# Optimization experiments

Hardware: AMD Instinct MI355X
Metric: run time of the kernel (lower is better)

The kernel has to match this reference:

```python
import jax, jax.numpy as jnp
import numpy as np

DIM = 1024
DEPTH = 3
BATCH = 8
SEQ = DIM  # module requires seq_len == dim for the residual add to broadcast


def setup_inputs() -> dict:
    key = jax.random.key(0)
    k1, k2, k3, k4 = jax.random.split(key, 4)
    x = jax.random.normal(k1, (BATCH, SEQ, DIM), dtype=jnp.float32)
    # torch.nn.Linear(dim, 3*dim): weight [3*dim, dim], bias [3*dim]
    Wqkv = jax.random.normal(k2, (3 * DIM, DIM), dtype=jnp.float32) * (1.0 / np.sqrt(DIM))
    bqkv = jax.random.normal(k3, (3 * DIM,), dtype=jnp.float32) * 0.01
    # self.w: Parameter of shape [depth, dim, dim], init randn
    w = jax.random.normal(k4, (DEPTH, DIM, DIM), dtype=jnp.float32)
    return {"x": x, "Wqkv": Wqkv, "bqkv": bqkv, "w": w}


def reference(x, Wqkv, bqkv, w):
    # qkv projection then chunk into q, k, v along last dim
    qkv = x @ Wqkv.T + bqkv                      # [B, S, 3*dim]
    q, k, v = jnp.split(qkv, 3, axis=-1)         # each [B, S, dim]
    scale = 1.0 / (q.shape[-1] ** 0.5)
    # sum over depth of (q @ w[i]) @ k^T, accumulated onto v
    # einsum contracts d (dim), e (dim), and sums over n (depth) in one pass
    scores = jnp.einsum('bsd,nde,bte->bst', q, w, k)  # [B, S, S]; requires S == dim
    return v + scores * scale
```

## Files before the change

kernel.cpp:

```cpp
#include <hip/hip_runtime.h>
#include <hip/hip_bf16.h>
#include <stdint.h>

typedef __bf16 bf16_t;
typedef __bf16 bf16x8 __attribute__((ext_vector_type(8)));
typedef __bf16 bf16x4 __attribute__((ext_vector_type(4)));
typedef float  f32x4  __attribute__((ext_vector_type(4)));

#define DIM   1024
#define BATCH 8
#define NTOK  (BATCH * DIM)
#define SCALE 0.03125f

__global__ __launch_bounds__(256)
void k_prep(const float* __restrict__ x, const float* __restrict__ Wqkv,
            const float* __restrict__ w,
            bf16_t* __restrict__ xb, bf16_t* __restrict__ wbig,
            bf16_t* __restrict__ wtb, bf16_t* __restrict__ wqt)
{
    __shared__ float tile[32][33];
    const int b = blockIdx.x;
    if (b < 8192) {
        const int i = b * 256 + threadIdx.x;
        const float4 v = reinterpret_cast<const float4*>(x)[i];
        bf16x4 o;
        o.x = (bf16_t)v.x; o.y = (bf16_t)v.y; o.z = (bf16_t)v.z; o.w = (bf16_t)v.w;
        reinterpret_cast<bf16x4*>(xb)[i] = o;
    } else if (b < 10240) {
        const int i = (b - 8192) * 256 + threadIdx.x;
        const float4 v = reinterpret_cast<const float4*>(Wqkv + 1048576)[i];
        bf16x4 o;
        o.x = (bf16_t)v.x; o.y = (bf16_t)v.y; o.z = (bf16_t)v.z; o.w = (bf16_t)v.w;
        reinterpret_cast<bf16x4*>(wbig + 1048576)[i] = o;
    } else if (b < 11264) {
        const int t  = b - 10240;
        const int tx = threadIdx.x & 31, ty = threadIdx.x >> 5;
        const int d0 = (t & 31) * 32, e0 = (t >> 5) * 32;
#pragma unroll
        for (int r = 0; r < 4; ++r) {
            const int d = d0 + r * 8 + ty;
            const int e = e0 + tx;
            tile[r * 8 + ty][tx] =
                w[d * 1024 + e] + w[1048576 + d * 1024 + e] + w[2097152 + d * 1024 + e];
        }
        __syncthreads();
#pragma unroll
        for (int r = 0; r < 4; ++r) {
            const int e = e0 + r * 8 + ty;
            const int d = d0 + tx;
            wtb[e * 1024 + d] = (bf16_t)tile[tx][r * 8 + ty];
        }
    } else {
        const int t  = b - 11264;
        const int tx = threadIdx.x & 31, ty = threadIdx.x >> 5;
        const int e0 = (t & 31) * 32, d0 = (t >> 5) * 32;
#pragma unroll
        for (int r = 0; r < 4; ++r)
            tile[r * 8 + ty][tx] = Wqkv[(long)(e0 + r * 8 + ty) * 1024 + d0 + tx];
        __syncthreads();
#pragma unroll
        for (int r = 0; r < 4; ++r)
            wqt[(long)(d0 + r * 8 + ty) * 1024 + e0 + tx] = (bf16_t)tile[tx][r * 8 + ty];
    }
}

__global__ __launch_bounds__(256)
void k_mid(const float* __restrict__ bq, const bf16_t* __restrict__ wtb,
           const bf16_t* __restrict__ wqt, float* __restrict__ bqwO,
           float* __restrict__ oP)
{
    __shared__ __align__(16) bf16_t As[128 * 32];
    __shared__ __align__(16) bf16_t Bs[128 * 32];

    const int tid  = threadIdx.x;
    const int wave = tid >> 6;
    const int lane = tid & 63;

    if (blockIdx.x < 256) {
        const int n = blockIdx.x * 4 + wave;
        const bf16_t* row = wtb + (long)n * 1024;
        float s = 0.f;
#pragma unroll
        for (int c = 0; c < 2; ++c) {
            const int d0 = (lane + c * 64) * 8;
            const bf16x8 v = *reinterpret_cast<const bf16x8*>(row + d0);
#pragma unroll
            for (int e = 0; e < 8; ++e) s += bq[d0 + e] * (float)v[e];
        }
#pragma unroll
        for (int off = 32; off; off >>= 1) s += __shfl_down(s, off);
        if (lane == 0) bqwO[n] = s;
        return;
    }

    const int s  = blockIdx.x - 256;
    const int bm = (s >> 5) * 128;
    const int bn = ((s >> 2) & 7) * 128;
    const int kb = (s & 3) * 256;
    float* outP  = oP + (long)(s & 3) * 1048576;
    const int wr = wave >> 1, wc = wave & 1;
    const int lhi = lane >> 4, llo = lane & 15;

    f32x4 acc[4][4];
    const f32x4 fz = {0.f, 0.f, 0.f, 0.f};
#pragma unroll
    for (int i = 0; i < 4; ++i)
#pragma unroll
        for (int j = 0; j < 4; ++j) acc[i][j] = fz;

    for (int k0 = 0; k0 < 256; k0 += 32) {
#pragma unroll
        for (int i = 0; i < 2; ++i) {
            const int c  = wave * 128 + i * 64 + lane;
            const int r  = c >> 2;
            const int cc = (c & 3) << 3;
            const long ga = (long)(bm + r) * 1024 + kb + k0 + cc;
            const long gb = (long)(bn + r) * 1024 + kb + k0 + cc;
            const int lbase = (wave * 128 + i * 64) << 3;
            __builtin_amdgcn_global_load_lds(
                (const __attribute__((address_space(1))) uint32_t*)(wtb + ga),
                (__attribute__((address_space(3))) uint32_t*)(&As[lbase]), 16, 0, 0);
            __builtin_amdgcn_global_load_lds(
                (const __attribute__((address_space(1))) uint32_t*)(wqt + gb),
                (__attribute__((address_space(3))) uint32_t*)(&Bs[lbase]), 16, 0, 0);
        }
        __syncthreads();

        bf16x8 af[4], bfr[4];
#pragma unroll
        for (int mi = 0; mi < 4; ++mi)
            af[mi] = *reinterpret_cast<const bf16x8*>(&As[(wr * 64 + mi * 16 + llo) * 32 + lhi * 8]);
#pragma unroll
        for (int ni = 0; ni < 4; ++ni)
            bfr[ni] = *reinterpret_cast<const bf16x8*>(&Bs[(wc * 64 + ni * 16 + llo) * 32 + lhi * 8]);
#pragma unroll
        for (int mi = 0; mi < 4; ++mi)
#pragma unroll
            for (int ni = 0; ni < 4; ++ni)
                acc[mi][ni] = __builtin_amdgcn_mfma_f32_16x16x32_bf16(af[mi], bfr[ni], acc[mi][ni], 0, 0, 0);
        __syncthreads();
    }

#pragma unroll
    for (int mi = 0; mi < 4; ++mi) {
        const int r0 = bm + wr * 64 + mi * 16 + lhi * 4;
#pragma unroll
        for (int ni = 0; ni < 4; ++ni) {
            const int cg = bn + wc * 64 + ni * 16 + llo;
            const f32x4 v = acc[mi][ni];
#pragma unroll
            for (int j = 0; j < 4; ++j)
                outP[(long)(r0 + j) * 1024 + cg] = v[j];
        }
    }
}

__global__ __launch_bounds__(256)
void k_cvt4(const float* __restrict__ p, bf16_t* __restrict__ out) {
    const int i = blockIdx.x * 256 + threadIdx.x;
    const f32x4* rp = reinterpret_cast<const f32x4*>(p);
    const f32x4 a = rp[i];
    const f32x4 b = rp[i + 262144];
    const f32x4 c = rp[i + 524288];
    const f32x4 d = rp[i + 786432];
    bf16x4 o;
    o.x = (bf16_t)(a.x + b.x + c.x + d.x);
    o.y = (bf16_t)(a.y + b.y + c.y + d.y);
    o.z = (bf16_t)(a.z + b.z + c.z + d.z);
    o.w = (bf16_t)(a.w + b.w + c.w + d.w);
    reinterpret_cast<bf16x4*>(out)[i] = o;
}

template<int BN_, int MODE>
__global__ __launch_bounds__(512, 2)
void k_db(const bf16_t* __restrict__ A, const bf16_t* __restrict__ Bp,
          const float* __restrict__ bqw, const float* __restrict__ bqkv,
          bf16_t* __restrict__ oQW, bf16_t* __restrict__ oK, float* __restrict__ oF)
{
    constexpr int NF   = BN_ / 64;
    constexpr int LB   = BN_ / 64;
    constexpr int LPT  = 2 + LB;
    constexpr int SLOT = (128 + BN_) * 128;
    constexpr int NTT  = 16;
    __shared__ __align__(16) unsigned char slds[2 * SLOT];

    const int tid  = threadIdx.x;
    const int wave = tid >> 6, lane = tid & 63;
    const int wm = wave >> 2, wn = wave & 3;
    const int llo = lane & 15, lhi = lane >> 4;

    int bm, bn; long zz = 0;
    if (MODE == 1) {
        bm = blockIdx.x * 128; bn = blockIdx.y * BN_;
    } else {
        const int nw = ((int)blockIdx.x & 7) * 64 + ((int)blockIdx.x >> 3);
        zz = (long)(nw >> 6) << 20;
        const int r = nw & 63;
        bm = (r >> 3) * 128; bn = (r & 7) * 128;
    }

    const bf16_t* sp[LPT]; int dst[LPT];
#pragma unroll
    for (int j = 0; j < 2; ++j) {
        const int C = j * 512 + tid;
        const int r = C >> 3, u = (C & 7) ^ (r & 7);
        sp[j] = A + zz + (long)(bm + r) * 1024 + (u << 3);
        dst[j] = C << 4;
    }
#pragma unroll
    for (int j = 0; j < LB; ++j) {
        const int C = j * 512 + tid;
        const int r = C >> 3, u = (C & 7) ^ (r & 7);
        sp[2 + j] = Bp + zz + (long)(bn + r) * 1024 + (u << 3);
        dst[2 + j] = 16384 + (C << 4);
    }

    auto stage = [&](int tt) {
        unsigned char* s = &slds[(tt & 1) * SLOT];
        const long ko = (long)tt << 6;
#pragma unroll
        for (int j = 0; j < LPT; ++j)
            __builtin_amdgcn_global_load_lds(
                (const __attribute__((address_space(1))) uint32_t*)(sp[j] + ko),
                (__attribute__((address_space(3))) uint32_t*)(s + dst[j]), 16, 0, 0);
    };

    f32x4 acc[4][NF];
    const f32x4 fz = {0.f, 0.f, 0.f, 0.f};
#pragma unroll
    for (int i = 0; i < 4; ++i)
#pragma unroll
        for (int j = 0; j < NF; ++j) acc[i][j] = fz;

    stage(0);

    for (int t = 0; t < NTT; ++t) {
        if (t + 1 < NTT) {
            stage(t + 1);
            asm volatile("s_waitcnt vmcnt(%0)" :: "i"(LPT) : "memory");
        } else {
            asm volatile("s_waitcnt vmcnt(0)" ::: "memory");
        }
        __builtin_amdgcn_s_barrier();

        const unsigned char* sb = &slds[(t & 1) * SLOT];
#pragma unroll
        for (int ks = 0; ks < 2; ++ks) {
            bf16x8 af[4], bfv[NF];
#pragma unroll
            for (int mi = 0; mi < 4; ++mi) {
                const int r = wm * 64 + mi * 16 + llo;
                af[mi] = *reinterpret_cast<const bf16x8*>(
                    sb + r * 128 + ((((ks << 2) | lhi) ^ (r & 7)) << 4));
            }
#pragma unroll
            for (int ni = 0; ni < NF; ++ni) {
                const int r = wn * (NF * 16) + ni * 16 + llo;
                bfv[ni] = *reinterpret_cast<const bf16x8*>(
                    sb + 16384 + r * 128 + ((((ks << 2) | lhi) ^ (r & 7)) << 4));
            }
            __builtin_amdgcn_s_setprio(1);
#pragma unroll
            for (int mi = 0; mi < 4; ++mi)
#pragma unroll
                for (int ni = 0; ni < NF; ++ni)
                    acc[mi][ni] = __builtin_amdgcn_mfma_f32_16x16x32_bf16(
                        af[mi], bfv[ni], acc[mi][ni], 0, 0, 0);
            __builtin_amdgcn_s_setprio(0);
        }
        asm volatile("s_waitcnt lgkmcnt(0)" ::: "memory");
        __builtin_amdgcn_s_barrier();
    }

#pragma unroll
    for (int mi = 0; mi < 4; ++mi) {
        const long r0 = bm + wm * 64 + mi * 16 + lhi * 4;
#pragma unroll
        for (int ni = 0; ni < NF; ++ni) {
            const int cg = bn + wn * (NF * 16) + ni * 16 + llo;
            const f32x4 v = acc[mi][ni];
            if (MODE == 1) {
                const int sec = cg >> 10;
                const int c1  = cg & 1023;
                const float bb = (sec == 0) ? bqw[cg] : bqkv[cg];
#pragma unroll
                for (int j = 0; j < 4; ++j) {
                    const long idx = (r0 + j) * 1024 + c1;
                    const float val = v[j] + bb;
                    if (sec == 0)      oQW[idx] = (bf16_t)val;
                    else if (sec == 1) oK[idx] = (bf16_t)val;
                    else               oF[idx] = val;
                }
            } else {
#pragma unroll
                for (int j = 0; j < 4; ++j) {
                    const long idx = zz + (r0 + j) * 1024 + cg;
                    oF[idx] = oF[idx] + SCALE * v[j];
                }
            }
        }
    }
}

extern "C" void kernel_launch(void* const* d_in, const int* in_sizes, int n_in,
                              void* d_out, int out_size, void* d_ws, size_t ws_size,
                              hipStream_t stream) {
    const float* x    = (const float*)d_in[0];
    const float* Wqkv = (const float*)d_in[1];
    const float* bqkv = (const float*)d_in[2];
    const float* w    = (const float*)d_in[3];
    float* out = (float*)d_out;

    char* ws = (char*)d_ws;
    bf16_t* xb   = (bf16_t*)(ws);
    bf16_t* wbig = (bf16_t*)(ws + (16l << 20));
    float*  bqw  = (float*) (ws + (22l << 20));
    bf16_t* kb   = (bf16_t*)(ws + (22l << 20) + 65536);
    float*  part = (float*) kb;
    bf16_t* qwb  = (bf16_t*)(ws + (38l << 20) + 65536);
    bf16_t* wtb  = qwb;
    bf16_t* wqt  = qwb + 1048576;
    if (ws_size < (size_t)(54l << 20) + 65536) return;

    k_prep<<<12288, 256, 0, stream>>>(x, Wqkv, w, xb, wbig, wtb, wqt);

    k_mid<<<512, 256, 0, stream>>>(bqkv, wtb, wqt, bqw, part);

    k_cvt4<<<1024, 256, 0, stream>>>(part, wbig);

    k_db<192, 1><<<dim3(64, 16), 512, 0, stream>>>(xb, wbig, bqw, bqkv, qwb, kb, out);

    k_db<128, 2><<<dim3(512), 512, 0, stream>>>(qwb, kb, nullptr, nullptr,
                                                nullptr, nullptr, out);
}
```

Measured before the change: 109.1 us.

## Reassociate score chain into a fused Wq^T·Weff·Wk matrix with rank-1 bias terms

Instead of projecting Q (folded with the summed depth weight), K and V and then multiplying QW by K^T, the code precomputes M = Wq^T·Weff·Wk with two small split-K GEMMs. It then computes T = x·M and forms scores plus V in one concatenated-K GEMM ([T | x] × [x | Wv]^T). Bias interactions are folded into per-row and per-column vectors (RU, RW, cO) and added in the epilogue. The goal is to cut total GEMM FLOPs and drop the separate K and QW intermediates, at the cost of more launches, extra rounding through a bf16 M, and altered numerics.

Result: slower. 112.2 us (+2.8%).

```diff
diff --git a/kernel.cpp b/kernel.cpp
--- a/kernel.cpp
+++ b/kernel.cpp
@@ -9,14 +9,96 @@
 
 #define DIM   1024
 #define BATCH 8
-#define NTOK  (BATCH * DIM)
 #define SCALE 0.03125f
+
+
+__device__ __forceinline__ float rowdot_bf16(const bf16_t* __restrict__ row,
+                                             const float* __restrict__ vec, int lane) {
+    float s = 0.f;
+#pragma unroll
+    for (int c = 0; c < 2; ++c) {
+        const int d0 = (lane + c * 64) * 8;
+        const bf16x8 v = *reinterpret_cast<const bf16x8*>(row + d0);
+#pragma unroll
+        for (int e = 0; e < 8; ++e) s += vec[d0 + e] * (float)v[e];
+    }
+#pragma unroll
+    for (int off = 32; off; off >>= 1) s += __shfl_down(s, off);
+    return s;
+}
+
+__device__ __forceinline__ void gemm_sk(const bf16_t* __restrict__ A, const bf16_t* __restrict__ B,
+                                        float* __restrict__ oP, int s, int tid,
+                                        bf16_t* As, bf16_t* Bs)
+{
+    const int wave = tid >> 6, lane = tid & 63;
+    const int bm = (s >> 5) * 128;
+    const int bn = ((s >> 2) & 7) * 128;
+    const int kb = (s & 3) * 256;
+    float* outP  = oP + (long)(s & 3) * 1048576;
+    const int wr = wave >> 1, wc = wave & 1;
+    const int lhi = lane >> 4, llo = lane & 15;
+
+    f32x4 acc[4][4];
+    const f32x4 fz = {0.f, 0.f, 0.f, 0.f};
+#pragma unroll
+    for (int i = 0; i < 4; ++i)
+#pragma unroll
+        for (int j = 0; j < 4; ++j) acc[i][j] = fz;
+
+    for (int k0 = 0; k0 < 256; k0 += 32) {
+#pragma unroll
+        for (int i = 0; i < 2; ++i) {
+            const int c  = wave * 128 + i * 64 + lane;
+            const int r  = c >> 2;
+            const int cc = (c & 3) << 3;
+            const long ga = (long)(bm + r) * 1024 + kb + k0 + cc;
+            const long gb = (long)(bn + r) * 1024 + kb + k0 + cc;
+            const int lbase = (wave * 128 + i * 64) << 3;
+            __builtin_amdgcn_global_load_lds(
+                (const __attribute__((address_space(1))) uint32_t*)(A + ga),
+                (__attribute__((address_space(3))) uint32_t*)(&As[lbase]), 16, 0, 0);
+            __builtin_amdgcn_global_load_lds(
+                (const __attribute__((address_space(1))) uint32_t*)(B + gb),
+                (__attribute__((address_space(3))) uint32_t*)(&Bs[lbase]), 16, 0, 0);
+        }
+        __syncthreads();
+
+        bf16x8 af[4], bfr[4];
+#pragma unroll
+        for (int mi = 0; mi < 4; ++mi)
+            af[mi] = *reinterpret_cast<const bf16x8*>(&As[(wr * 64 + mi * 16 + llo) * 32 + lhi * 8]);
+#pragma unroll
+        for (int ni = 0; ni < 4; ++ni)
+            bfr[ni] = *reinterpret_cast<const bf16x8*>(&Bs[(wc * 64 + ni * 16 + llo) * 32 + lhi * 8]);
+#pragma unroll
+        for (int mi = 0; mi < 4; ++mi)
+#pragma unroll
+            for (int ni = 0; ni < 4; ++ni)
+                acc[mi][ni] = __builtin_amdgcn_mfma_f32_16x16x32_bf16(af[mi], bfr[ni], acc[mi][ni], 0, 0, 0);
+        __syncthreads();
+    }
+
+#pragma unroll
+    for (int mi = 0; mi < 4; ++mi) {
+        const int r0 = bm + wr * 64 + mi * 16 + lhi * 4;
+#pragma unroll
+        for (int ni = 0; ni < 4; ++ni) {
+            const int cg = bn + wc * 64 + ni * 16 + llo;
+            const f32x4 v = acc[mi][ni];
+#pragma unroll
+            for (int j = 0; j < 4; ++j)
+                outP[(long)(r0 + j) * 1024 + cg] = v[j];
+        }
+    }
+}
 
 __global__ __launch_bounds__(256)
 void k_prep(const float* __restrict__ x, const float* __restrict__ Wqkv,
             const float* __restrict__ w,
-            bf16_t* __restrict__ xb, bf16_t* __restrict__ wbig,
-            bf16_t* __restrict__ wtb, bf16_t* __restrict__ wqt)
+            bf16_t* __restrict__ xb, bf16_t* __restrict__ wvb,
+            bf16_t* __restrict__ weff, bf16_t* __restrict__ wtb,
+            bf16_t* __restrict__ wqt, bf16_t* __restrict__ wkt)
 {
     __shared__ float tile[32][33];
     const int b = blockIdx.x;
@@ -26,162 +108,173 @@
         bf16x4 o;
         o.x = (bf16_t)v.x; o.y = (bf16_t)v.y; o.z = (bf16_t)v.z; o.w = (bf16_t)v.w;
         reinterpret_cast<bf16x4*>(xb)[i] = o;
-    } else if (b < 10240) {
+    } else if (b < 9216) {
         const int i = (b - 8192) * 256 + threadIdx.x;
-        const float4 v = reinterpret_cast<const float4*>(Wqkv + 1048576)[i];
+        const float4 v = reinterpret_cast<const float4*>(Wqkv + 2097152)[i];
         bf16x4 o;
         o.x = (bf16_t)v.x; o.y = (bf16_t)v.y; o.z = (bf16_t)v.z; o.w = (bf16_t)v.w;
-        reinterpret_cast<bf16x4*>(wbig + 1048576)[i] = o;
-    } else if (b < 11264) {
-        const int t  = b - 10240;
+        reinterpret_cast<bf16x4*>(wvb)[i] = o;
+    } else if (b < 10240) {
+        const int t  = b - 9216;
         const int tx = threadIdx.x & 31, ty = threadIdx.x >> 5;
         const int d0 = (t & 31) * 32, e0 = (t >> 5) * 32;
 #pragma unroll
         for (int r = 0; r < 4; ++r) {
             const int d = d0 + r * 8 + ty;
             const int e = e0 + tx;
-            tile[r * 8 + ty][tx] =
+            const float sum =
                 w[d * 1024 + e] + w[1048576 + d * 1024 + e] + w[2097152 + d * 1024 + e];
+            tile[r * 8 + ty][tx] = sum;
+            weff[(long)d * 1024 + e] = (bf16_t)sum;
         }
         __syncthreads();
 #pragma unroll
         for (int r = 0; r < 4; ++r) {
             const int e = e0 + r * 8 + ty;
             const int d = d0 + tx;
-            wtb[e * 1024 + d] = (bf16_t)tile[tx][r * 8 + ty];
+            wtb[(long)e * 1024 + d] = (bf16_t)tile[tx][r * 8 + ty];
         }
     } else {
-        const int t  = b - 11264;
+        const bool isQ = (b < 11264);
+        const int t  = b - (isQ ? 10240 : 11264);
+        const float* src = isQ ? Wqkv : (Wqkv + 1048576);
+        bf16_t* dst = isQ ? wqt : wkt;
         const int tx = threadIdx.x & 31, ty = threadIdx.x >> 5;
         const int e0 = (t & 31) * 32, d0 = (t >> 5) * 32;
 #pragma unroll
         for (int r = 0; r < 4; ++r)
-            tile[r * 8 + ty][tx] = Wqkv[(long)(e0 + r * 8 + ty) * 1024 + d0 + tx];
+            tile[r * 8 + ty][tx] = src[(long)(e0 + r * 8 + ty) * 1024 + d0 + tx];
         __syncthreads();
 #pragma unroll
         for (int r = 0; r < 4; ++r)
-            wqt[(long)(d0 + r * 8 + ty) * 1024 + e0 + tx] = (bf16_t)tile[tx][r * 8 + ty];
+            dst[(long)(d0 + r * 8 + ty) * 1024 + e0 + tx] = (bf16_t)tile[tx][r * 8 + ty];
     }
 }
 
 __global__ __launch_bounds__(256)
-void k_mid(const float* __restrict__ bq, const bf16_t* __restrict__ wtb,
-           const bf16_t* __restrict__ wqt, float* __restrict__ bqwO,
-           float* __restrict__ oP)
+void k_midA(const bf16_t* __restrict__ wkt, const bf16_t* __restrict__ weff,
+            const bf16_t* __restrict__ wtb, const float* __restrict__ bqkv,
+            float* __restrict__ pX1, float* __restrict__ h1, float* __restrict__ h2)
 {
     __shared__ __align__(16) bf16_t As[128 * 32];
     __shared__ __align__(16) bf16_t Bs[128 * 32];
-
-    const int tid  = threadIdx.x;
-    const int wave = tid >> 6;
-    const int lane = tid & 63;
-
     if (blockIdx.x < 256) {
-        const int n = blockIdx.x * 4 + wave;
-        const bf16_t* row = wtb + (long)n * 1024;
-        float s = 0.f;
-#pragma unroll
-        for (int c = 0; c < 2; ++c) {
-            const int d0 = (lane + c * 64) * 8;
-            const bf16x8 v = *reinterpret_cast<const bf16x8*>(row + d0);
-#pragma unroll
-            for (int e = 0; e < 8; ++e) s += bq[d0 + e] * (float)v[e];
-        }
-#pragma unroll
-        for (int off = 32; off; off >>= 1) s += __shfl_down(s, off);
-        if (lane == 0) bqwO[n] = s;
+        gemm_sk(wkt, weff, pX1, blockIdx.x, threadIdx.x, As, Bs);
         return;
     }
-
-    const int s  = blockIdx.x - 256;
-    const int bm = (s >> 5) * 128;
-    const int bn = ((s >> 2) & 7) * 128;
-    const int kb = (s & 3) * 256;
-    float* outP  = oP + (long)(s & 3) * 1048576;
-    const int wr = wave >> 1, wc = wave & 1;
-    const int lhi = lane >> 4, llo = lane & 15;
-
-    f32x4 acc[4][4];
-    const f32x4 fz = {0.f, 0.f, 0.f, 0.f};
-#pragma unroll
-    for (int i = 0; i < 4; ++i)
-#pragma unroll
-        for (int j = 0; j < 4; ++j) acc[i][j] = fz;
-
-    for (int k0 = 0; k0 < 256; k0 += 32) {
-#pragma unroll
-        for (int i = 0; i < 2; ++i) {
-            const int c  = wave * 128 + i * 64 + lane;
-            const int r  = c >> 2;
-            const int cc = (c & 3) << 3;
-            const long ga = (long)(bm + r) * 1024 + kb + k0 + cc;
-            const long gb = (long)(bn + r) * 1024 + kb + k0 + cc;
-            const int lbase = (wave * 128 + i * 64) << 3;
-            __builtin_amdgcn_global_load_lds(
-                (const __attribute__((address_space(1))) uint32_t*)(wtb + ga),
-                (__attribute__((address_space(3))) uint32_t*)(&As[lbase]), 16, 0, 0);
-            __builtin_amdgcn_global_load_lds(
-                (const __attribute__((address_space(1))) uint32_t*)(wqt + gb),
-                (__attribute__((address_space(3))) uint32_t*)(&Bs[lbase]), 16, 0, 0);
-        }
-        __syncthreads();
-
-        bf16x8 af[4], bfr[4];
-#pragma unroll
-        for (int mi = 0; mi < 4; ++mi)
-            af[mi] = *reinterpret_cast<const bf16x8*>(&As[(wr * 64 + mi * 16 + llo) * 32 + lhi * 8]);
-#pragma unroll
-        for (int ni = 0; ni < 4; ++ni)
-            bfr[ni] = *reinterpret_cast<const bf16x8*>(&Bs[(wc * 64 + ni * 16 + llo) * 32 + lhi * 8]);
-#pragma unroll
-        for (int mi = 0; mi < 4; ++mi)
-#pragma unroll
-            for (int ni = 0; ni < 4; ++ni)
-                acc[mi][ni] = __builtin_amdgcn_mfma_f32_16x16x32_bf16(af[mi], bfr[ni], acc[mi][ni], 0, 0, 0);
-        __syncthreads();
-    }
-
-#pragma unroll
-    for (int mi = 0; mi < 4; ++mi) {
-        const int r0 = bm + wr * 64 + mi * 16 + lhi * 4;
-#pragma unroll
-        for (int ni = 0; ni < 4; ++ni) {
-            const int cg = bn + wc * 64 + ni * 16 + llo;
-            const f32x4 v = acc[mi][ni];
-#pragma unroll
-            for (int j = 0; j < 4; ++j)
-                outP[(long)(r0 + j) * 1024 + cg] = v[j];
-        }
+    const int wave = threadIdx.x >> 6, lane = threadIdx.x & 63;
+    const int r = ((int)blockIdx.x - 256) * 4 + wave;
+    if (r < 1024) {
+        const float s = rowdot_bf16(weff + (long)r * 1024, bqkv + 1024, lane);
+        if (lane == 0) h1[r] = s;
+    } else {
+        const float s = rowdot_bf16(wtb + (long)(r - 1024) * 1024, bqkv, lane);
+        if (lane == 0) h2[r - 1024] = s;
     }
 }
 
 __global__ __launch_bounds__(256)
-void k_cvt4(const float* __restrict__ p, bf16_t* __restrict__ out) {
+void k_cvtA(const float* __restrict__ p, bf16_t* __restrict__ X1b,
+            const bf16_t* __restrict__ wqt, const bf16_t* __restrict__ wkt,
+            const float* __restrict__ h1, const float* __restrict__ h2,
+            const float* __restrict__ bqkv,
+            float* __restrict__ u, float* __restrict__ w2, float* __restrict__ cO)
+{
+    const int b = blockIdx.x;
+    if (b < 1024) {
+        const int i = b * 256 + threadIdx.x;
+        const f32x4* rp = reinterpret_cast<const f32x4*>(p);
+        const f32x4 a0 = rp[i], a1 = rp[i + 262144], a2 = rp[i + 524288], a3 = rp[i + 786432];
+        bf16x4 o;
+        o.x = (bf16_t)(a0.x + a1.x + a2.x + a3.x);
+        o.y = (bf16_t)(a0.y + a1.y + a2.y + a3.y);
+        o.z = (bf16_t)(a0.z + a1.z + a2.z + a3.z);
+        o.w = (bf16_t)(a0.w + a1.w + a2.w + a3.w);
+        reinterpret_cast<bf16x4*>(X1b)[i] = o;
+    } else if (b < 1536) {
+        const int wave = threadIdx.x >> 6, lane = threadIdx.x & 63;
+        const int rr = (b - 1024) * 4 + wave;
+        if (rr < 1024) {
+            const float s = rowdot_bf16(wqt + (long)rr * 1024, h1, lane);
+            if (lane == 0) u[rr] = s;
+        } else {
+            const float s = rowdot_bf16(wkt + (long)(rr - 1024) * 1024, h2, lane);
+            if (lane == 0) w2[rr - 1024] = s;
+        }
+    } else {
+        if (threadIdx.x < 64) {
+            float s = 0.f;
+            for (int i = threadIdx.x; i < 1024; i += 64) s += bqkv[i] * h1[i];
+#pragma unroll
+            for (int off = 32; off; off >>= 1) s += __shfl_down(s, off);
+            if (threadIdx.x == 0) cO[0] = s;
+        }
+    }
+}
+
+__global__ __launch_bounds__(256)
+void k_midB(const bf16_t* __restrict__ X1b, const bf16_t* __restrict__ wqt,
+            float* __restrict__ pMT, const bf16_t* __restrict__ xb,
+            const float* __restrict__ u, const float* __restrict__ w2,
+            const float* __restrict__ cO,
+            float* __restrict__ RU, float* __restrict__ RW)
+{
+    __shared__ __align__(16) bf16_t As[128 * 32];
+    __shared__ __align__(16) bf16_t Bs[128 * 32];
+    if (blockIdx.x < 256) {
+        gemm_sk(X1b, wqt, pMT, blockIdx.x, threadIdx.x, As, Bs);
+        return;
+    }
+    const int wave = threadIdx.x >> 6, lane = threadIdx.x & 63;
+    const int s = ((int)blockIdx.x - 256) * 4 + wave;
+    const bf16_t* row = xb + (long)s * 1024;
+    float s1 = 0.f, s2 = 0.f;
+#pragma unroll
+    for (int c = 0; c < 2; ++c) {
+        const int d0 = (lane + c * 64) * 8;
+        const bf16x8 v = *reinterpret_cast<const bf16x8*>(row + d0);
+#pragma unroll
+        for (int e = 0; e < 8; ++e) {
+            const float f = (float)v[e];
+            s1 += u[d0 + e] * f;
+            s2 += w2[d0 + e] * f;
+        }
+    }
+#pragma unroll
+    for (int off = 32; off; off >>= 1) { s1 += __shfl_down(s1, off); s2 += __shfl_down(s2, off); }
+    if (lane == 0) {
+        RU[s] = SCALE * (s1 + cO[0]);
+        RW[s] = SCALE * s2;
+    }
+}
+
+__global__ __launch_bounds__(256)
+void k_cvtS(const float* __restrict__ p, bf16_t* __restrict__ out) {
     const int i = blockIdx.x * 256 + threadIdx.x;
     const f32x4* rp = reinterpret_cast<const f32x4*>(p);
-    const f32x4 a = rp[i];
-    const f32x4 b = rp[i + 262144];
-    const f32x4 c = rp[i + 524288];
-    const f32x4 d = rp[i + 786432];
+    const f32x4 a0 = rp[i], a1 = rp[i + 262144], a2 = rp[i + 524288], a3 = rp[i + 786432];
     bf16x4 o;
-    o.x = (bf16_t)(a.x + b.x + c.x + d.x);
-    o.y = (bf16_t)(a.y + b.y + c.y + d.y);
-    o.z = (bf16_t)(a.z + b.z + c.z + d.z);
-    o.w = (bf16_t)(a.w + b.w + c.w + d.w);
+    o.x = (bf16_t)(SCALE * (a0.x + a1.x + a2.x + a3.x));
+    o.y = (bf16_t)(SCALE * (a0.y + a1.y + a2.y + a3.y));
+    o.z = (bf16_t)(SCALE * (a0.z + a1.z + a2.z + a3.z));
+    o.w = (bf16_t)(SCALE * (a0.w + a1.w + a2.w + a3.w));
     reinterpret_cast<bf16x4*>(out)[i] = o;
 }
 
-template<int BN_, int MODE>
+#define GLOAD(SRC, DST) __builtin_amdgcn_global_load_lds( \
+    (const __attribute__((address_space(1))) uint32_t*)(SRC), \
+    (__attribute__((address_space(3))) uint32_t*)(DST), 16, 0, 0)
+
+template<int MODE>
 __global__ __launch_bounds__(512, 2)
-void k_db(const bf16_t* __restrict__ A, const bf16_t* __restrict__ Bp,
-          const float* __restrict__ bqw, const float* __restrict__ bqkv,
-          bf16_t* __restrict__ oQW, bf16_t* __restrict__ oK, float* __restrict__ oF)
-{
-    constexpr int NF   = BN_ / 64;
-    constexpr int LB   = BN_ / 64;
-    constexpr int LPT  = 2 + LB;
-    constexpr int SLOT = (128 + BN_) * 128;
-    constexpr int NTT  = 16;
+void k_db2(const bf16_t* __restrict__ A1, const bf16_t* __restrict__ A2,
+           const bf16_t* __restrict__ B1, const bf16_t* __restrict__ B2,
+           const float* __restrict__ RUv, const float* __restrict__ RWv,
+           const float* __restrict__ bv,
+           bf16_t* __restrict__ oT, float* __restrict__ oF)
+{
+    constexpr int SLOT = 32768;
+    constexpr int NTT  = (MODE == 0) ? 16 : 32;
     __shared__ __align__(16) unsigned char slds[2 * SLOT];
 
     const int tid  = threadIdx.x;
@@ -189,55 +282,55 @@
     const int wm = wave >> 2, wn = wave & 3;
     const int llo = lane & 15, lhi = lane >> 4;
 
-    int bm, bn; long zz = 0;
-    if (MODE == 1) {
-        bm = blockIdx.x * 128; bn = blockIdx.y * BN_;
+    int bm, bn, z = 0;
+    if (MODE == 0) {
+        bm = ((int)blockIdx.x >> 3) * 128;
+        bn = ((int)blockIdx.x & 7) * 128;
     } else {
         const int nw = ((int)blockIdx.x & 7) * 64 + ((int)blockIdx.x >> 3);
-        zz = (long)(nw >> 6) << 20;
+        z = nw >> 6;
         const int r = nw & 63;
         bm = (r >> 3) * 128; bn = (r & 7) * 128;
     }
-
-    const bf16_t* sp[LPT]; int dst[LPT];
+    const long zo = (long)z << 20;
+
+    const bf16_t *sA1[2], *sB1[2], *sA2[2], *sB2[2];
+    int dA[2], dB[2];
 #pragma unroll
     for (int j = 0; j < 2; ++j) {
         const int C = j * 512 + tid;
         const int r = C >> 3, u = (C & 7) ^ (r & 7);
-        sp[j] = A + zz + (long)(bm + r) * 1024 + (u << 3);
-        dst[j] = C << 4;
-    }
-#pragma unroll
-    for (int j = 0; j < LB; ++j) {
-        const int C = j * 512 + tid;
-        const int r = C >> 3, u = (C & 7) ^ (r & 7);
-        sp[2 + j] = Bp + zz + (long)(bn + r) * 1024 + (u << 3);
-        dst[2 + j] = 16384 + (C << 4);
+        const long aoff = (long)(bm + r) * 1024 + (u << 3);
+        const long boff = (long)(bn + r) * 1024 + (u << 3);
+        sA1[j] = A1 + zo + aoff;  dA[j] = C << 4;
+        sB1[j] = B1 + zo + boff;  dB[j] = 16384 + (C << 4);
+        if (MODE == 1) { sA2[j] = A2 + zo + aoff; sB2[j] = B2 + boff; }
     }
 
     auto stage = [&](int tt) {
         unsigned char* s = &slds[(tt & 1) * SLOT];
-        const long ko = (long)tt << 6;
-#pragma unroll
-        for (int j = 0; j < LPT; ++j)
-            __builtin_amdgcn_global_load_lds(
-                (const __attribute__((address_space(1))) uint32_t*)(sp[j] + ko),
-                (__attribute__((address_space(3))) uint32_t*)(s + dst[j]), 16, 0, 0);
+        const long ko = (long)(tt & 15) << 6;
+        const bool hB = (MODE == 1) && (tt >= 16);
+#pragma unroll
+        for (int j = 0; j < 2; ++j) {
+            GLOAD((hB ? sA2[j] : sA1[j]) + ko, s + dA[j]);
+            GLOAD((hB ? sB2[j] : sB1[j]) + ko, s + dB[j]);
+        }
     };
 
-    f32x4 acc[4][NF];
+    f32x4 acc[4][2];
     const f32x4 fz = {0.f, 0.f, 0.f, 0.f};
 #pragma unroll
     for (int i = 0; i < 4; ++i)
 #pragma unroll
-        for (int j = 0; j < NF; ++j) acc[i][j] = fz;
+        for (int j = 0; j < 2; ++j) acc[i][j] = fz;
 
     stage(0);
 
     for (int t = 0; t < NTT; ++t) {
         if (t + 1 < NTT) {
             stage(t + 1);
-            asm volatile("s_waitcnt vmcnt(%0)" :: "i"(LPT) : "memory");
+            asm volatile("s_waitcnt vmcnt(4)" ::: "memory");
         } else {
             asm volatile("s_waitcnt vmcnt(0)" ::: "memory");
         }
@@ -246,7 +339,7 @@
         const unsigned char* sb = &slds[(t & 1) * SLOT];
 #pragma unroll
         for (int ks = 0; ks < 2; ++ks) {
-            bf16x8 af[4], bfv[NF];
+            bf16x8 af[4], bfv[2];
 #pragma unroll
             for (int mi = 0; mi < 4; ++mi) {
                 const int r = wm * 64 + mi * 16 + llo;
@@ -254,8 +347,8 @@
                     sb + r * 128 + ((((ks << 2) | lhi) ^ (r & 7)) << 4));
             }
 #pragma unroll
-            for (int ni = 0; ni < NF; ++ni) {
-                const int r = wn * (NF * 16) + ni * 16 + llo;
+            for (int ni = 0; ni < 2; ++ni) {
+                const int r = wn * 32 + ni * 16 + llo;
                 bfv[ni] = *reinterpret_cast<const bf16x8*>(
                     sb + 16384 + r * 128 + ((((ks << 2) | lhi) ^ (r & 7)) << 4));
             }
@@ -263,7 +356,7 @@
 #pragma unroll
             for (int mi = 0; mi < 4; ++mi)
 #pragma unroll
-                for (int ni = 0; ni < NF; ++ni)
+                for (int ni = 0; ni < 2; ++ni)
                     acc[mi][ni] = __builtin_amdgcn_mfma_f32_16x16x32_bf16(
                         af[mi], bfv[ni], acc[mi][ni], 0, 0, 0);
             __builtin_amdgcn_s_setprio(0);
@@ -274,33 +367,27 @@
 
 #pragma unroll
     for (int mi = 0; mi < 4; ++mi) {
-        const long r0 = bm + wm * 64 + mi * 16 + lhi * 4;
-#pragma unroll
-        for (int ni = 0; ni < NF; ++ni) {
-            const int cg = bn + wn * (NF * 16) + ni * 16 + llo;
+        const int lr0 = bm + wm * 64 + mi * 16 + lhi * 4;
+#pragma unroll
+        for (int ni = 0; ni < 2; ++ni) {
+            const int cg = bn + wn * 32 + ni * 16 + llo;
             const f32x4 v = acc[mi][ni];
-            if (MODE == 1) {
-                const int sec = cg >> 10;
-                const int c1  = cg & 1023;
-                const float bb = (sec == 0) ? bqw[cg] : bqkv[cg];
+            if (MODE == 0) {
+#pragma unroll
+                for (int j = 0; j < 4; ++j)
+                    oT[(long)(lr0 + j) * 1024 + cg] = (bf16_t)v[j];
+            } else {
+                const float cterm = RWv[z * 1024 + cg] + bv[cg];
 #pragma unroll
                 for (int j = 0; j < 4; ++j) {
-                    const long idx = (r0 + j) * 1024 + c1;
-                    const float val = v[j] + bb;
-                    if (sec == 0)      oQW[idx] = (bf16_t)val;
-                    else if (sec == 1) oK[idx] = (bf16_t)val;
-                    else               oF[idx] = val;
-                }
-            } else {
-#pragma unroll
-                for (int j = 0; j < 4; ++j) {
-                    const long idx = zz + (r0 + j) * 1024 + cg;
-                    oF[idx] = oF[idx] + SCALE * v[j];
+                    const int lr = lr0 + j;
+                    oF[zo + (long)lr * 1024 + cg] = v[j] + RUv[z * 1024 + lr] + cterm;
                 }
             }
         }
     }
 }
+#undef GLOAD
 
 extern "C" void kernel_launch(void* const* d_in, const int* in_sizes, int n_in,
                               void* d_out, int out_size, void* d_ws, size_t ws_size,
@@ -312,24 +399,39 @@
     float* out = (float*)d_out;
 
     char* ws = (char*)d_ws;
-    bf16_t* xb   = (bf16_t*)(ws);
-    bf16_t* wbig = (bf16_t*)(ws + (16l << 20));
-    float*  bqw  = (float*) (ws + (22l << 20));
-    bf16_t* kb   = (bf16_t*)(ws + (22l << 20) + 65536);
-    float*  part = (float*) kb;
-    bf16_t* qwb  = (bf16_t*)(ws + (38l << 20) + 65536);
-    bf16_t* wtb  = qwb;
-    bf16_t* wqt  = qwb + 1048576;
+    bf16_t* xb   = (bf16_t*)ws;
+    float*  pbig = (float*) (ws + (16l << 20));
+    bf16_t* tsb  = (bf16_t*)(ws + (16l << 20));
+    bf16_t* weff = (bf16_t*)(ws + (32l << 20));
+    bf16_t* wtb  = (bf16_t*)(ws + (34l << 20));
+    bf16_t* wqt  = (bf16_t*)(ws + (36l << 20));
+    bf16_t* wkt  = (bf16_t*)(ws + (38l << 20));
+    bf16_t* wvb  = (bf16_t*)(ws + (40l << 20));
+    bf16_t* X1b  = (bf16_t*)(ws + (42l << 20));
+    bf16_t* MTb  = (bf16_t*)(ws + (44l << 20));
+    char*   sm   = ws + (46l << 20);
+    float* h1 = (float*)sm;
+    float* h2 = (float*)(sm + 4096);
+    float* u  = (float*)(sm + 8192);
+    float* w2 = (float*)(sm + 12288);
+    float* cO = (float*)(sm + 16384);
+    float* RU = (float*)(sm + 20480);
+    float* RW = (float*)(sm + 53248);
     if (ws_size < (size_t)(54l << 20) + 65536) return;
 
-    k_prep<<<12288, 256, 0, stream>>>(x, Wqkv, w, xb, wbig, wtb, wqt);
-
-    k_mid<<<512, 256, 0, stream>>>(bqkv, wtb, wqt, bqw, part);
-
-    k_cvt4<<<1024, 256, 0, stream>>>(part, wbig);
-
-    k_db<192, 1><<<dim3(64, 16), 512, 0, stream>>>(xb, wbig, bqw, bqkv, qwb, kb, out);
-
-    k_db<128, 2><<<dim3(512), 512, 0, stream>>>(qwb, kb, nullptr, nullptr,
-                                                nullptr, nullptr, out);
-}
+    k_prep<<<12288, 256, 0, stream>>>(x, Wqkv, w, xb, wvb, weff, wtb, wqt, wkt);
+
+    k_midA<<<768, 256, 0, stream>>>(wkt, weff, wtb, bqkv, pbig, h1, h2);
+
+    k_cvtA<<<1537, 256, 0, stream>>>(pbig, X1b, wqt, wkt, h1, h2, bqkv, u, w2, cO);
+
+    k_midB<<<2304, 256, 0, stream>>>(X1b, wqt, pbig, xb, u, w2, cO, RU, RW);
+
+    k_cvtS<<<1024, 256, 0, stream>>>(pbig, MTb);
+
+    k_db2<0><<<512, 512, 0, stream>>>(xb, nullptr, MTb, nullptr,
+                                      nullptr, nullptr, nullptr, tsb, nullptr);
+
+    k_db2<1><<<512, 512, 0, stream>>>(tsb, xb, xb, wvb,
+                                      RU, RW, bqkv + 2048, nullptr, out);
+}
```
